# Performance work log

Measured on AMD Instinct MI355X. Metric: run time of the kernel, lower is better.

Reference implementation:

```python
import jax, jax.numpy as jnp
import numpy as np

N_NODES = 100000
N_EDGES = 1000000
VOCAB = 5000
EMBED = 64
HIDDEN = 128
N_CLASSES = 16
N_GRAPHS = 8192


def setup_inputs() -> dict:
    key = jax.random.key(0)
    ks = jax.random.split(key, 10)
    node_ids = jax.random.randint(ks[0], (N_NODES,), 0, VOCAB)
    edge_index = jax.random.randint(ks[1], (2, N_EDGES), 0, N_NODES)
    batch = jnp.sort(jax.random.randint(ks[2], (N_NODES,), 0, N_GRAPHS))
    embed = jax.random.normal(ks[3], (VOCAB, EMBED), jnp.float32) * 0.02
    embed = embed.at[0].set(0.0)  # padding_idx=0
    W1 = jax.random.normal(ks[4], (EMBED, HIDDEN), jnp.float32) / np.sqrt(EMBED)
    b1 = jnp.zeros((HIDDEN,), jnp.float32)
    W2 = jax.random.normal(ks[5], (HIDDEN, HIDDEN), jnp.float32) / np.sqrt(HIDDEN)
    b2 = jnp.zeros((HIDDEN,), jnp.float32)
    Wout = jax.random.normal(ks[6], (HIDDEN, N_CLASSES), jnp.float32) / np.sqrt(HIDDEN)
    bout = jnp.zeros((N_CLASSES,), jnp.float32)
    return dict(node_ids=node_ids, edge_index=edge_index, batch=batch,
                embed=embed, W1=W1, b1=b1, W2=W2, b2=b2, Wout=Wout, bout=bout)


def reference(node_ids, edge_index, batch, embed, W1, b1, W2, b2, Wout, bout):
    N = node_ids.shape[0]
    # embedding lookup
    x = embed[node_ids]  # [N, EMBED]
    # GCNConv default: add self-loops + symmetric D^{-1/2} (A+I) D^{-1/2} normalization
    loop = jnp.arange(N)
    src = jnp.concatenate([edge_index[0], loop])  # [E+N]
    dst = jnp.concatenate([edge_index[1], loop])
    deg = jax.ops.segment_sum(jnp.ones_like(src, jnp.float32), dst, num_segments=N)
    dinv = jax.lax.rsqrt(jnp.maximum(deg, 1.0))  # deg>=1 due to self-loops
    norm = (dinv[src] * dinv[dst])[:, None]  # [E+N, 1]

    def gcn(h, W, b):
        h = h @ W  # transform first (PyG order), then propagate
        msg = h[src] * norm  # gather + scale
        agg = jax.ops.segment_sum(msg, dst, num_segments=N)  # scatter-add
        return agg + b

    x = jax.nn.relu(gcn(x, W1, b1))
    x = jax.nn.relu(gcn(x, W2, b2))
    # global mean pool over graphs
    counts = jax.ops.segment_sum(jnp.ones((N,), jnp.float32), batch, num_segments=N_GRAPHS)
    pooled = jax.ops.segment_sum(x, batch, num_segments=N_GRAPHS) / jnp.maximum(counts, 1.0)[:, None]
    return pooled @ Wout + bout  # [N_GRAPHS, N_CLASSES]
```

## Files before the change

### kernel.cpp

```cpp
#include <hip/hip_runtime.h>
#include <hip/hip_fp16.h>

#define HID 128
#define EMB 64
#define NG  8192
#define NCLS 16
#define SCAN_T 4096
#define MMB 64
#define SRCBITS 17
#define SMASK ((1u << SRCBITS) - 1)

typedef _Float16 f16x8 __attribute__((ext_vector_type(8)));
typedef float    f32x4 __attribute__((ext_vector_type(4)));

__device__ __forceinline__ void fma8(float* a, uint4 r, float w) {
    const _Float16* h = (const _Float16*)&r;
#pragma unroll
    for (int k = 0; k < 8; ++k) a[k] = fmaf((float)h[k], w, a[k]);
}

__global__ void k_degprep(const int* __restrict__ dst, int E,
                          int* __restrict__ deg, int* __restrict__ epos,
                          const float* __restrict__ embed, const float* __restrict__ W1,
                          const float* __restrict__ W2, const int* __restrict__ batch,
                          __half* __restrict__ xw, __half* __restrict__ wt2,
                          int* __restrict__ gstart, int V, int N, int degB, int xwB) {
    int b = (int)blockIdx.x;
    if (b < degB) {
        int i = b * 256 + threadIdx.x;
        if (i < E) epos[i] = atomicAdd(&deg[dst[i]], 1);
    } else if (b < degB + xwB) {
        int v = ((b - degB) * 256 + threadIdx.x) >> 6;
        if (v >= V) return;
        int lane = threadIdx.x & 63;
        float ev = embed[(size_t)v * EMB + lane];
        float a0 = 0.f, a1 = 0.f;
#pragma unroll
        for (int k = 0; k < EMB; ++k) {
            float e = __shfl(ev, k, 64);
            float2 w = *(const float2*)&W1[k * HID + 2 * lane];
            a0 = fmaf(e, w.x, a0);
            a1 = fmaf(e, w.y, a1);
        }
        ((__half2*)xw)[(size_t)v * 64 + lane] = __floats2half2_rn(a0, a1);
    } else if (b < degB + xwB + 64) {
        int i = (b - degB - xwB) * 256 + threadIdx.x;
        int c = i >> 7, k = i & 127;
        wt2[i] = __float2half(W2[k * HID + c]);
    } else {
        int n = (b - degB - xwB - 64) * 256 + threadIdx.x;
        if (n > N) return;
        int bc = (n < N) ? batch[n] : NG;
        int bp = (n > 0) ? batch[n - 1] : -1;
        for (int g = bp + 1; g <= bc; ++g) gstart[g] = n;
    }
}

__global__ void k_scanA(const int* __restrict__ deg, int* __restrict__ tsum, int N, int seg) {
    int t = blockIdx.x * 256 + threadIdx.x;
    int beg = t * seg, end = min(beg + seg, N);
    int s = 0;
    for (int i = beg; i < end; ++i) s += deg[i];
    tsum[t] = s;
}

__global__ void k_scanB(int* __restrict__ tsum) {
    __shared__ int sh[256];
    int tid = threadIdx.x;
    const int PER = SCAN_T / 256;
    int vals[PER];
    int local = 0;
    int base = tid * PER;
#pragma unroll
    for (int i = 0; i < PER; ++i) { vals[i] = tsum[base + i]; local += vals[i]; }
    sh[tid] = local; __syncthreads();
    for (int d = 1; d < 256; d <<= 1) {
        int v = (tid >= d) ? sh[tid - d] : 0;
        __syncthreads();
        sh[tid] += v;
        __syncthreads();
    }
    int off = sh[tid] - local;
#pragma unroll
    for (int i = 0; i < PER; ++i) { int v = vals[i]; tsum[base + i] = off; off += v; }
}

__global__ void k_scanC(const int* __restrict__ deg, const int* __restrict__ tsum,
                        int* __restrict__ rowptr, float* __restrict__ dinv,
                        int N, int seg, int E) {
    int t = blockIdx.x * 256 + threadIdx.x;
    int beg = t * seg, end = min(beg + seg, N);
    int off = tsum[t];
    for (int i = beg; i < end; ++i) {
        int dg = deg[i];
        rowptr[i] = off; off += dg;
        dinv[i] = rsqrtf((float)(dg + 1));
    }
    if (t == 0) rowptr[N] = E;
}

__global__ void k_fill(const int* __restrict__ src, const int* __restrict__ dst,
                       const int* __restrict__ ids, const int* __restrict__ rowptr,
                       const int* __restrict__ epos, unsigned* __restrict__ csr32, int E) {
    int e4 = (blockIdx.x * 256 + threadIdx.x) * 4;
    if (e4 + 4 <= E) {
        int4 s4 = *(const int4*)&src[e4];
        int4 d4 = *(const int4*)&dst[e4];
        int4 p4 = *(const int4*)&epos[e4];
        csr32[rowptr[d4.x] + p4.x] = ((unsigned)ids[s4.x] << SRCBITS) | (unsigned)s4.x;
        csr32[rowptr[d4.y] + p4.y] = ((unsigned)ids[s4.y] << SRCBITS) | (unsigned)s4.y;
        csr32[rowptr[d4.z] + p4.z] = ((unsigned)ids[s4.z] << SRCBITS) | (unsigned)s4.z;
        csr32[rowptr[d4.w] + p4.w] = ((unsigned)ids[s4.w] << SRCBITS) | (unsigned)s4.w;
    } else {
        for (int e = e4; e < E; ++e) {
            int s = src[e], d = dst[e];
            csr32[rowptr[d] + epos[e]] = ((unsigned)ids[s] << SRCBITS) | (unsigned)s;
        }
    }
}

__global__ void k_gather1(const int* __restrict__ ids, const __half* __restrict__ xw,
                          const unsigned* __restrict__ csr32, const int* __restrict__ rowptr,
                          const float* __restrict__ dinv, const float* __restrict__ bias,
                          __half* __restrict__ h1, int N) {
    int wid = (blockIdx.x * blockDim.x + threadIdx.x) >> 6;
    int lane = threadIdx.x & 63;
    int half = lane >> 5;
    int d = wid * 2 + half;
    bool act = d < N;
    int dc = act ? d : N - 1;
    int eg = (lane >> 4) & 1;
    unsigned cb = (unsigned)(lane & 15) << 4;
    int2 rp = *(const int2*)&rowptr[dc];
    int beg = rp.x, end = rp.y;
    float dd = dinv[dc];
    const char* xwb = (const char*)xw;
    float a[8] = {0.f, 0.f, 0.f, 0.f, 0.f, 0.f, 0.f, 0.f};
    if (eg == 0) {
        uint4 r = *(const uint4*)(xwb + (((unsigned)ids[dc] << 8) | cb));
        fma8(a, r, dd);
    }
    for (int i = beg; i < end; i += 8) {
        float w[4]; unsigned ro[4]; uint4 r[4];
#pragma unroll
        for (int j = 0; j < 4; ++j) {
            int idx = i + 2 * j + eg;
            bool v = idx < end;
            unsigned p = csr32[v ? idx : beg];
            w[j] = v ? dinv[p & SMASK] : 0.f;
            ro[j] = v ? (((p >> SRCBITS) << 8) | cb) : cb;
        }
#pragma unroll
        for (int j = 0; j < 4; ++j) r[j] = *(const uint4*)(xwb + ro[j]);
#pragma unroll
        for (int j = 0; j < 4; ++j) fma8(a, r[j], w[j]);
    }
#pragma unroll
    for (int k = 0; k < 8; ++k) a[k] += __shfl_xor(a[k], 16, 64);
    if (eg == 0 && act) {
        int c = lane & 15;
        float4 bl = *(const float4*)&bias[c * 8];
        float4 bh = *(const float4*)&bias[c * 8 + 4];
        __half2 h0 = __floats2half2_rn(fmaxf(fmaf(a[0], dd, bl.x), 0.f),
                                       fmaxf(fmaf(a[1], dd, bl.y), 0.f));
        __half2 h1v = __floats2half2_rn(fmaxf(fmaf(a[2], dd, bl.z), 0.f),
                                        fmaxf(fmaf(a[3], dd, bl.w), 0.f));
        __half2 h2v = __floats2half2_rn(fmaxf(fmaf(a[4], dd, bh.x), 0.f),
                                        fmaxf(fmaf(a[5], dd, bh.y), 0.f));
        __half2 h3 = __floats2half2_rn(fmaxf(fmaf(a[6], dd, bh.z), 0.f),
                                       fmaxf(fmaf(a[7], dd, bh.w), 0.f));
        uint4 pk = make_uint4(*(unsigned*)&h0, *(unsigned*)&h1v,
                              *(unsigned*)&h2v, *(unsigned*)&h3);
        ((uint4*)(h1 + (size_t)dc * HID))[c] = pk;
    }
}

__global__ __launch_bounds__(256) void k_mm2_mfma(const __half* __restrict__ h1,
                                                  const __half* __restrict__ wt,
                                                  const float* __restrict__ dinv,
                                                  __half* __restrict__ h2, int N) {
    int tid = threadIdx.x;
    int w = tid >> 6, l = tid & 63;
    int base = blockIdx.x * MMB + w * 16;
    int lrow = l & 15, lkg = l >> 4;
    int node = base + lrow;
    int nc = node < N ? node : N - 1;
    const f16x8* ap = (const f16x8*)(h1 + (size_t)nc * HID);
    f16x8 a0 = ap[0 * 4 + lkg], a1 = ap[1 * 4 + lkg];
    f16x8 a2 = ap[2 * 4 + lkg], a3 = ap[3 * 4 + lkg];
    f32x4 acc[8];
#pragma unroll
    for (int ct = 0; ct < 8; ++ct) acc[ct] = (f32x4){0.f, 0.f, 0.f, 0.f};
    const f16x8* wp = (const f16x8*)wt;
#pragma unroll
    for (int ct = 0; ct < 8; ++ct) {
        const f16x8* bp = wp + (ct * 16 + lrow) * 16 + lkg;
        f16x8 b0 = bp[0], b1 = bp[4], b2 = bp[8], b3 = bp[12];
        acc[ct] = __builtin_amdgcn_mfma_f32_16x16x32_f16(b0, a0, acc[ct], 0, 0, 0);
        acc[ct] = __builtin_amdgcn_mfma_f32_16x16x32_f16(b1, a1, acc[ct], 0, 0, 0);
        acc[ct] = __builtin_amdgcn_mfma_f32_16x16x32_f16(b2, a2, acc[ct], 0, 0, 0);
        acc[ct] = __builtin_amdgcn_mfma_f32_16x16x32_f16(b3, a3, acc[ct], 0, 0, 0);
    }
    if (node < N) {
        float sc = dinv[node];
#pragma unroll
        for (int ct = 0; ct < 8; ++ct) {
            int wc = ct * 16 + lkg * 4;
            __half2 lo = __floats2half2_rn(acc[ct][0] * sc, acc[ct][1] * sc);
            __half2 hi = __floats2half2_rn(acc[ct][2] * sc, acc[ct][3] * sc);
            uint2 pk = make_uint2(*(unsigned*)&lo, *(unsigned*)&hi);
            *(uint2*)&h2[(size_t)node * HID + wc] = pk;
        }
    }
}

__global__ void k_gather2(const __half* __restrict__ h2, const unsigned* __restrict__ csr32,
                          const int* __restrict__ rowptr, const float* __restrict__ dinv,
                          const float* __restrict__ bias, __half* __restrict__ x2, int N) {
    int wid = (blockIdx.x * blockDim.x + threadIdx.x) >> 6;
    int lane = threadIdx.x & 63;
    int half = lane >> 5;
    int d = wid * 2 + half;
    bool act = d < N;
    int dc = act ? d : N - 1;
    int eg = (lane >> 4) & 1;
    unsigned cb = (unsigned)(lane & 15) << 4;
    int2 rp = *(const int2*)&rowptr[dc];
    int beg = rp.x, end = rp.y;
    float dd = dinv[dc];
    const char* hb = (const char*)h2;
    float a[8] = {0.f, 0.f, 0.f, 0.f, 0.f, 0.f, 0.f, 0.f};
    if (eg == 0) {
        uint4 r = *(const uint4*)(hb + (((unsigned)dc << 8) | cb));
        fma8(a, r, 1.f);
    }
    for (int i = beg; i < end; i += 8) {
        float w[4]; unsigned ro[4]; uint4 r[4];
#pragma unroll
        for (int j = 0; j < 4; ++j) {
            int idx = i + 2 * j + eg;
            bool v = idx < end;
            unsigned p = csr32[v ? idx : beg];
            w[j] = v ? 1.f : 0.f;
            ro[j] = v ? (((p & SMASK) << 8) | cb) : cb;
        }
#pragma unroll
        for (int j = 0; j < 4; ++j) r[j] = *(const uint4*)(hb + ro[j]);
#pragma unroll
        for (int j = 0; j < 4; ++j) fma8(a, r[j], w[j]);
    }
#pragma unroll
    for (int k = 0; k < 8; ++k) a[k] += __shfl_xor(a[k], 16, 64);
    if (eg == 0 && act) {
        int c = lane & 15;
        float4 bl = *(const float4*)&bias[c * 8];
        float4 bh = *(const float4*)&bias[c * 8 + 4];
        __half2 h0 = __floats2half2_rn(fmaxf(fmaf(a[0], dd, bl.x), 0.f),
                                       fmaxf(fmaf(a[1], dd, bl.y), 0.f));
        __half2 h1v = __floats2half2_rn(fmaxf(fmaf(a[2], dd, bl.z), 0.f),
                                        fmaxf(fmaf(a[3], dd, bl.w), 0.f));
        __half2 h2v = __floats2half2_rn(fmaxf(fmaf(a[4], dd, bh.x), 0.f),
                                        fmaxf(fmaf(a[5], dd, bh.y), 0.f));
        __half2 h3 = __floats2half2_rn(fmaxf(fmaf(a[6], dd, bh.z), 0.f),
                                       fmaxf(fmaf(a[7], dd, bh.w), 0.f));
        uint4 pk = make_uint4(*(unsigned*)&h0, *(unsigned*)&h1v,
                              *(unsigned*)&h2v, *(unsigned*)&h3);
        ((uint4*)(x2 + (size_t)dc * HID))[c] = pk;
    }
}

__global__ void k_poolhead(const __half* __restrict__ x2, const int* __restrict__ gstart,
                           const float* __restrict__ Wout, const float* __restrict__ bout,
                           float* __restrict__ out) {
    int g = (blockIdx.x * blockDim.x + threadIdx.x) >> 6;
    if (g >= NG) return;
    int lane = threadIdx.x & 63;
    int beg = gstart[g], end = gstart[g + 1];
    const __half2* rows = (const __half2*)x2;
    float sx = 0.f, sy = 0.f;
    for (int n = beg; n < end; ++n) {
        float2 v = __half22float2(rows[(size_t)n * 64 + lane]);
        sx += v.x; sy += v.y;
    }
    float inv = (end > beg) ? 1.f / (float)(end - beg) : 1.f;
    sx *= inv; sy *= inv;
    float wo0[NCLS], wo1[NCLS];
    {
        const float4* p0 = (const float4*)&Wout[(size_t)(2 * lane) * NCLS];
        const float4* p1 = (const float4*)&Wout[(size_t)(2 * lane + 1) * NCLS];
#pragma unroll
        for (int j = 0; j < 4; ++j) {
            float4 a = p0[j]; wo0[4*j] = a.x; wo0[4*j+1] = a.y; wo0[4*j+2] = a.z; wo0[4*j+3] = a.w;
            float4 c = p1[j]; wo1[4*j] = c.x; wo1[4*j+1] = c.y; wo1[4*j+2] = c.z; wo1[4*j+3] = c.w;
        }
    }
#pragma unroll
    for (int c = 0; c < NCLS; ++c) {
        float p = fmaf(sx, wo0[c], sy * wo1[c]);
#pragma unroll
        for (int s = 1; s < 64; s <<= 1) p += __shfl_xor(p, s, 64);
        if (lane == c) out[(size_t)g * NCLS + c] = p + bout[c];
    }
}

static inline size_t align_up(size_t v, size_t a) { return (v + a - 1) & ~(a - 1); }

extern "C" void kernel_launch(void* const* d_in, const int* in_sizes, int n_in,
                              void* d_out, int out_size, void* d_ws, size_t ws_size,
                              hipStream_t stream) {
    const int*   node_ids = (const int*)d_in[0];
    const int*   edge     = (const int*)d_in[1];
    const int*   batch    = (const int*)d_in[2];
    const float* embed    = (const float*)d_in[3];
    const float* W1       = (const float*)d_in[4];
    const float* b1       = (const float*)d_in[5];
    const float* W2       = (const float*)d_in[6];
    const float* b2       = (const float*)d_in[7];
    const float* Wout     = (const float*)d_in[8];
    const float* bout     = (const float*)d_in[9];
    float* out = (float*)d_out;

    const int N = in_sizes[0];
    const int E = in_sizes[1] / 2;
    const int V = in_sizes[3] / EMB;
    const int seg = (N + SCAN_T - 1) / SCAN_T;

    char* wsb = (char*)d_ws;
    size_t off = 0;
    float*    dinv   = (float*)(wsb + off);    off = align_up(off + (size_t)N * 4, 256);
    int*      deg    = (int*)(wsb + off);      off = align_up(off + (size_t)N * 4, 256);
    int*      rowptr = (int*)(wsb + off);      off = align_up(off + (size_t)(N + 1) * 4, 256);
    int*      tsum   = (int*)(wsb + off);      off = align_up(off + (size_t)SCAN_T * 4, 256);
    int*      gstart = (int*)(wsb + off);      off = align_up(off + (size_t)(NG + 1) * 4, 256);
    __half*   wt2    = (__half*)(wsb + off);   off = align_up(off + (size_t)HID * HID * 2, 256);
    __half*   xw     = (__half*)(wsb + off);   off = align_up(off + (size_t)V * HID * 2, 256);
    int*      epos   = (int*)(wsb + off);      off = align_up(off + (size_t)E * 4, 256);
    unsigned* csr32  = (unsigned*)(wsb + off); off = align_up(off + (size_t)E * 4, 256);
    __half*   h1     = (__half*)(wsb + off);   off = align_up(off + (size_t)N * HID * 2, 256);
    __half*   h2     = (__half*)(wsb + off);   off = align_up(off + (size_t)N * HID * 2, 256);
    __half*   x2     = (__half*)(wsb + off);   off = align_up(off + (size_t)N * HID * 2, 256);

    const int* src = edge;
    const int* dst = edge + E;

    hipMemsetAsync(deg, 0, (size_t)N * 4, stream);
    {
        int degB = (E + 255) / 256;
        int xwB  = (V * 64 + 255) / 256;
        int bndB = (N + 1 + 255) / 256;
        k_degprep<<<degB + xwB + 64 + bndB, 256, 0, stream>>>(
            dst, E, deg, epos, embed, W1, W2, batch, xw, wt2, gstart, V, N, degB, xwB);
    }
    k_scanA<<<SCAN_T / 256, 256, 0, stream>>>(deg, tsum, N, seg);
    k_scanB<<<1, 256, 0, stream>>>(tsum);
    k_scanC<<<SCAN_T / 256, 256, 0, stream>>>(deg, tsum, rowptr, dinv, N, seg, E);
    k_fill<<<(E / 4 + 255) / 256, 256, 0, stream>>>(src, dst, node_ids, rowptr, epos, csr32, E);

    const int NW = (N + 1) / 2;

    k_gather1<<<(NW * 64 + 255) / 256, 256, 0, stream>>>(node_ids, xw, csr32, rowptr,
                                                         dinv, b1, h1, N);

    k_mm2_mfma<<<(N + MMB - 1) / MMB, 256, 0, stream>>>(h1, wt2, dinv, h2, N);
    k_gather2<<<(NW * 64 + 255) / 256, 256, 0, stream>>>(h2, csr32, rowptr, dinv, b2, x2, N);

    k_poolhead<<<(NG * 64 + 255) / 256, 256, 0, stream>>>(x2, gstart, Wout, bout, out);
}
```

Baseline: 229.0 us.

## Split degree atomics into vectorized kernel with padded counters; map 4 nodes per wave in gathers

```diff
diff --git a/kernel.cpp b/kernel.cpp
--- a/kernel.cpp
+++ b/kernel.cpp
@@ -19,18 +19,30 @@
     for (int k = 0; k < 8; ++k) a[k] = fmaf((float)h[k], w, a[k]);
 }
 
-__global__ void k_degprep(const int* __restrict__ dst, int E,
-                          int* __restrict__ deg, int* __restrict__ epos,
-                          const float* __restrict__ embed, const float* __restrict__ W1,
-                          const float* __restrict__ W2, const int* __restrict__ batch,
-                          __half* __restrict__ xw, __half* __restrict__ wt2,
-                          int* __restrict__ gstart, int V, int N, int degB, int xwB) {
+__global__ void k_deg(const int* __restrict__ dst, int E, int* __restrict__ deg4,
+                      int* __restrict__ epos) {
+    int e4 = (blockIdx.x * 256 + threadIdx.x) * 4;
+    if (e4 + 4 <= E) {
+        int4 d4 = *(const int4*)&dst[e4];
+        int4 p;
+        p.x = atomicAdd(&deg4[(size_t)d4.x * 4], 1);
+        p.y = atomicAdd(&deg4[(size_t)d4.y * 4], 1);
+        p.z = atomicAdd(&deg4[(size_t)d4.z * 4], 1);
+        p.w = atomicAdd(&deg4[(size_t)d4.w * 4], 1);
+        *(int4*)&epos[e4] = p;
+    } else {
+        for (int e = e4; e < E; ++e)
+            epos[e] = atomicAdd(&deg4[(size_t)dst[e] * 4], 1);
+    }
+}
+
+__global__ void k_prep(const float* __restrict__ embed, const float* __restrict__ W1,
+                       const float* __restrict__ W2, const int* __restrict__ batch,
+                       __half* __restrict__ xw, __half* __restrict__ wt2,
+                       int* __restrict__ gstart, int V, int N, int xwB) {
     int b = (int)blockIdx.x;
-    if (b < degB) {
-        int i = b * 256 + threadIdx.x;
-        if (i < E) epos[i] = atomicAdd(&deg[dst[i]], 1);
-    } else if (b < degB + xwB) {
-        int v = ((b - degB) * 256 + threadIdx.x) >> 6;
+    if (b < xwB) {
+        int v = (b * 256 + threadIdx.x) >> 6;
         if (v >= V) return;
         int lane = threadIdx.x & 63;
         float ev = embed[(size_t)v * EMB + lane];
@@ -43,12 +55,12 @@
             a1 = fmaf(e, w.y, a1);
         }
         ((__half2*)xw)[(size_t)v * 64 + lane] = __floats2half2_rn(a0, a1);
-    } else if (b < degB + xwB + 64) {
-        int i = (b - degB - xwB) * 256 + threadIdx.x;
+    } else if (b < xwB + 64) {
+        int i = (b - xwB) * 256 + threadIdx.x;
         int c = i >> 7, k = i & 127;
         wt2[i] = __float2half(W2[k * HID + c]);
     } else {
-        int n = (b - degB - xwB - 64) * 256 + threadIdx.x;
+        int n = (b - xwB - 64) * 256 + threadIdx.x;
         if (n > N) return;
         int bc = (n < N) ? batch[n] : NG;
         int bp = (n > 0) ? batch[n - 1] : -1;
@@ -56,11 +68,11 @@
     }
 }
 
-__global__ void k_scanA(const int* __restrict__ deg, int* __restrict__ tsum, int N, int seg) {
+__global__ void k_scanA(const int* __restrict__ deg4, int* __restrict__ tsum, int N, int seg) {
     int t = blockIdx.x * 256 + threadIdx.x;
     int beg = t * seg, end = min(beg + seg, N);
     int s = 0;
-    for (int i = beg; i < end; ++i) s += deg[i];
+    for (int i = beg; i < end; ++i) s += deg4[(size_t)i * 4];
     tsum[t] = s;
 }
 
@@ -85,14 +97,14 @@
     for (int i = 0; i < PER; ++i) { int v = vals[i]; tsum[base + i] = off; off += v; }
 }
 
-__global__ void k_scanC(const int* __restrict__ deg, const int* __restrict__ tsum,
+__global__ void k_scanC(const int* __restrict__ deg4, const int* __restrict__ tsum,
                         int* __restrict__ rowptr, float* __restrict__ dinv,
                         int N, int seg, int E) {
     int t = blockIdx.x * 256 + threadIdx.x;
     int beg = t * seg, end = min(beg + seg, N);
     int off = tsum[t];
     for (int i = beg; i < end; ++i) {
-        int dg = deg[i];
+        int dg = deg4[(size_t)i * 4];
         rowptr[i] = off; off += dg;
         dinv[i] = rsqrtf((float)(dg + 1));
     }
@@ -125,26 +137,25 @@
                           __half* __restrict__ h1, int N) {
     int wid = (blockIdx.x * blockDim.x + threadIdx.x) >> 6;
     int lane = threadIdx.x & 63;
-    int half = lane >> 5;
-    int d = wid * 2 + half;
+    int q = lane >> 4;
+    int d = wid * 4 + q;
     bool act = d < N;
     int dc = act ? d : N - 1;
-    int eg = (lane >> 4) & 1;
     unsigned cb = (unsigned)(lane & 15) << 4;
     int2 rp = *(const int2*)&rowptr[dc];
     int beg = rp.x, end = rp.y;
     float dd = dinv[dc];
     const char* xwb = (const char*)xw;
     float a[8] = {0.f, 0.f, 0.f, 0.f, 0.f, 0.f, 0.f, 0.f};
-    if (eg == 0) {
+    {
         uint4 r = *(const uint4*)(xwb + (((unsigned)ids[dc] << 8) | cb));
         fma8(a, r, dd);
     }
-    for (int i = beg; i < end; i += 8) {
+    for (int i = beg; i < end; i += 4) {
         float w[4]; unsigned ro[4]; uint4 r[4];
 #pragma unroll
         for (int j = 0; j < 4; ++j) {
-            int idx = i + 2 * j + eg;
+            int idx = i + j;
             bool v = idx < end;
             unsigned p = csr32[v ? idx : beg];
             w[j] = v ? dinv[p & SMASK] : 0.f;
@@ -155,9 +166,7 @@
 #pragma unroll
         for (int j = 0; j < 4; ++j) fma8(a, r[j], w[j]);
     }
-#pragma unroll
-    for (int k = 0; k < 8; ++k) a[k] += __shfl_xor(a[k], 16, 64);
-    if (eg == 0 && act) {
+    if (act) {
         int c = lane & 15;
         float4 bl = *(const float4*)&bias[c * 8];
         float4 bh = *(const float4*)&bias[c * 8 + 4];
@@ -219,26 +228,25 @@
                           const float* __restrict__ bias, __half* __restrict__ x2, int N) {
     int wid = (blockIdx.x * blockDim.x + threadIdx.x) >> 6;
     int lane = threadIdx.x & 63;
-    int half = lane >> 5;
-    int d = wid * 2 + half;
+    int q = lane >> 4;
+    int d = wid * 4 + q;
     bool act = d < N;
     int dc = act ? d : N - 1;
-    int eg = (lane >> 4) & 1;
     unsigned cb = (unsigned)(lane & 15) << 4;
     int2 rp = *(const int2*)&rowptr[dc];
     int beg = rp.x, end = rp.y;
     float dd = dinv[dc];
     const char* hb = (const char*)h2;
     float a[8] = {0.f, 0.f, 0.f, 0.f, 0.f, 0.f, 0.f, 0.f};
-    if (eg == 0) {
+    {
         uint4 r = *(const uint4*)(hb + (((unsigned)dc << 8) | cb));
         fma8(a, r, 1.f);
     }
-    for (int i = beg; i < end; i += 8) {
+    for (int i = beg; i < end; i += 4) {
         float w[4]; unsigned ro[4]; uint4 r[4];
 #pragma unroll
         for (int j = 0; j < 4; ++j) {
-            int idx = i + 2 * j + eg;
+            int idx = i + j;
             bool v = idx < end;
             unsigned p = csr32[v ? idx : beg];
             w[j] = v ? 1.f : 0.f;
@@ -249,9 +257,7 @@
 #pragma unroll
         for (int j = 0; j < 4; ++j) fma8(a, r[j], w[j]);
     }
-#pragma unroll
-    for (int k = 0; k < 8; ++k) a[k] += __shfl_xor(a[k], 16, 64);
-    if (eg == 0 && act) {
+    if (act) {
         int c = lane & 15;
         float4 bl = *(const float4*)&bias[c * 8];
         float4 bh = *(const float4*)&bias[c * 8 + 4];
@@ -328,7 +334,7 @@
     char* wsb = (char*)d_ws;
     size_t off = 0;
     float*    dinv   = (float*)(wsb + off);    off = align_up(off + (size_t)N * 4, 256);
-    int*      deg    = (int*)(wsb + off);      off = align_up(off + (size_t)N * 4, 256);
+    int*      deg4   = (int*)(wsb + off);      off = align_up(off + (size_t)N * 16, 256);
     int*      rowptr = (int*)(wsb + off);      off = align_up(off + (size_t)(N + 1) * 4, 256);
     int*      tsum   = (int*)(wsb + off);      off = align_up(off + (size_t)SCAN_T * 4, 256);
     int*      gstart = (int*)(wsb + off);      off = align_up(off + (size_t)(NG + 1) * 4, 256);
@@ -343,20 +349,20 @@
     const int* src = edge;
     const int* dst = edge + E;
 
-    hipMemsetAsync(deg, 0, (size_t)N * 4, stream);
+    hipMemsetAsync(deg4, 0, (size_t)N * 16, stream);
+    k_deg<<<(E / 4 + 255) / 256, 256, 0, stream>>>(dst, E, deg4, epos);
     {
-        int degB = (E + 255) / 256;
         int xwB  = (V * 64 + 255) / 256;
         int bndB = (N + 1 + 255) / 256;
-        k_degprep<<<degB + xwB + 64 + bndB, 256, 0, stream>>>(
-            dst, E, deg, epos, embed, W1, W2, batch, xw, wt2, gstart, V, N, degB, xwB);
-    }
-    k_scanA<<<SCAN_T / 256, 256, 0, stream>>>(deg, tsum, N, seg);
+        k_prep<<<xwB + 64 + bndB, 256, 0, stream>>>(embed, W1, W2, batch,
+                                                    xw, wt2, gstart, V, N, xwB);
+    }
+    k_scanA<<<SCAN_T / 256, 256, 0, stream>>>(deg4, tsum, N, seg);
     k_scanB<<<1, 256, 0, stream>>>(tsum);
-    k_scanC<<<SCAN_T / 256, 256, 0, stream>>>(deg, tsum, rowptr, dinv, N, seg, E);
+    k_scanC<<<SCAN_T / 256, 256, 0, stream>>>(deg4, tsum, rowptr, dinv, N, seg, E);
     k_fill<<<(E / 4 + 255) / 256, 256, 0, stream>>>(src, dst, node_ids, rowptr, epos, csr32, E);
 
-    const int NW = (N + 1) / 2;
+    const int NW = (N + 3) / 4;
 
     k_gather1<<<(NW * 64 + 255) / 256, 256, 0, stream>>>(node_ids, xw, csr32, rowptr,
                                                          dinv, b1, h1, N);
```

Result: faster. 221.2 us (-3.4%).
